# Optimization experiments

Hardware: AMD Instinct MI355X
Metric: run time of the kernel (lower is better)

The kernel has to match this reference:

```python
import jax, jax.numpy as jnp
import numpy as np

N_HEAD = 16
HEAD_DIM = 64  # n_embd // n_head = 1024 // 16

def setup_inputs() -> dict:
    key = jax.random.key(0)
    k1, k2, k3 = jax.random.split(key, 3)
    B, T, C = 4, 2048, 1024
    x = jax.random.normal(k1, (B, T, C), dtype=jnp.float32)
    w_qkv = jax.random.normal(k2, (3 * C, C), dtype=jnp.float32) * (C ** -0.5)
    w_proj = jax.random.normal(k3, (C, C), dtype=jnp.float32) * (C ** -0.5)
    b_proj = jnp.zeros((C,), dtype=jnp.float32)
    return {"x": x, "w_qkv": w_qkv, "w_proj": w_proj, "b_proj": b_proj}

def reference(x, w_qkv, w_proj, b_proj):
    B, T, C = x.shape
    H, hd = N_HEAD, HEAD_DIM
    # fused QKV projection (no bias), torch Linear: x @ W^T
    qkv = jnp.einsum('btc,dc->btd', x, w_qkv)           # [B,T,3C]
    # module-specific reshape: per-head groups of 3*hd, then chunk into q,k,v
    qkv = qkv.reshape(B, T, H, 3 * hd)
    q, k, v = jnp.split(qkv, 3, axis=-1)                # each [B,T,H,hd]
    q = q.transpose(0, 2, 1, 3)                         # [B,H,T,hd]
    k = k.transpose(0, 2, 1, 3)
    v = v.transpose(0, 2, 1, 3)
    att = jnp.einsum('bhqd,bhkd->bhqk', q, k) * (hd ** -0.5)
    causal = jnp.tril(jnp.ones((T, T), dtype=bool))
    att = jnp.where(causal, att, -jnp.inf)
    att = jax.nn.softmax(att, axis=-1)
    out = jnp.einsum('bhqk,bhkd->bhqd', att, v)         # [B,H,T,hd]
    out = out.transpose(0, 2, 1, 3).reshape(B, T, C)
    out = jnp.einsum('btc,dc->btd', out, w_proj) + b_proj
    return out
```

## Files before the change

kernel.cpp:

```cpp
#include <hip/hip_runtime.h>
#include <hip/hip_bf16.h>

typedef __attribute__((ext_vector_type(8))) short bf16x8;
typedef __attribute__((ext_vector_type(4))) float f32x4;
typedef __attribute__((ext_vector_type(16))) float f32x16;
typedef __attribute__((ext_vector_type(4))) int i32x4;
typedef unsigned short u16;

__device__ __forceinline__ u16 f2bf(float f) {
    __hip_bfloat16 h = __float2bfloat16(f);
    return __builtin_bit_cast(u16, h);
}
__device__ __forceinline__ bf16x8 load8(const u16* p) {
    return *reinterpret_cast<const bf16x8*>(p);
}
__device__ __forceinline__ void gl2lds16(const u16* g, u16* l) {
    __builtin_amdgcn_global_load_lds(
        (const __attribute__((address_space(1))) void*)g,
        (__attribute__((address_space(3))) void*)l, 16, 0, 0);
}
__device__ __forceinline__ unsigned int cvtpk(float lo, float hi) {
    unsigned int r;
    asm("v_cvt_pk_bf16_f32 %0, %1, %2" : "=v"(r) : "v"(lo), "v"(hi));
    return r;
}

#define QSCALE 0.1803368801111244f

__global__ __launch_bounds__(256) void cast_f32_bf16(
    const float* __restrict__ src, u16* __restrict__ dst, int n4)
{
    int i = blockIdx.x * blockDim.x + threadIdx.x;
    if (i < n4) {
        float4 f = reinterpret_cast<const float4*>(src)[i];
        ushort4 o;
        o.x = f2bf(f.x); o.y = f2bf(f.y); o.z = f2bf(f.z); o.w = f2bf(f.w);
        reinterpret_cast<ushort4*>(dst)[i] = o;
    }
}

#define GEMM128_BODY(EPILOGUE)                                                 \
    __shared__ __align__(16) u16 As[128 * 32];                                 \
    __shared__ __align__(16) u16 Bs[128 * 32];                                 \
    const int t = threadIdx.x;                                                 \
    const int lane = t & 63;                                                   \
    const int wave = t >> 6;                                                   \
    const int quad = lane >> 4;                                                \
    const int lid  = lane & 15;                                                \
    const int wrow = wave & 1;                                                 \
    const int wcol = wave >> 1;                                                \
    const int mtile = blockIdx.x * 128;                                        \
    const int ntile = blockIdx.y * 128;                                        \
    const int srow = t >> 2;                                                   \
    const int scol = (t & 3) * 8;                                              \
    const u16* ga0 = Aptr + (size_t)(mtile + srow) * 1024 + scol;              \
    const u16* ga1 = Aptr + (size_t)(mtile + 64 + srow) * 1024 + scol;         \
    const u16* gb0 = Bptr + (size_t)(ntile + srow) * 1024 + scol;              \
    const u16* gb1 = Bptr + (size_t)(ntile + 64 + srow) * 1024 + scol;         \
    u16* la0 = As + t * 8;                                                     \
    u16* la1 = As + (256 + t) * 8;                                             \
    u16* lb0 = Bs + t * 8;                                                     \
    u16* lb1 = Bs + (256 + t) * 8;                                             \
    f32x4 acc[4][4] = {};                                                      \
    const int aro = wrow * 64 * 32 + quad * 8;                                 \
    const int bro = wcol * 64 * 32 + quad * 8;                                 \
    for (int k0 = 0; k0 < 1024; k0 += 32) {                                    \
        __syncthreads();                                                       \
        gl2lds16(ga0 + k0, la0);                                               \
        gl2lds16(ga1 + k0, la1);                                               \
        gl2lds16(gb0 + k0, lb0);                                               \
        gl2lds16(gb1 + k0, lb1);                                               \
        __syncthreads();                                                       \
        bf16x8 a[4], b[4];                                                     \
        _Pragma("unroll")                                                      \
        for (int i = 0; i < 4; ++i) {                                          \
            a[i] = load8(As + aro + (i * 16 + lid) * 32);                      \
            b[i] = load8(Bs + bro + (i * 16 + lid) * 32);                      \
        }                                                                      \
        _Pragma("unroll")                                                      \
        for (int mi = 0; mi < 4; ++mi)                                         \
            _Pragma("unroll")                                                  \
            for (int ni = 0; ni < 4; ++ni)                                     \
                acc[mi][ni] = __builtin_amdgcn_mfma_f32_16x16x32_bf16(         \
                    a[mi], b[ni], acc[mi][ni], 0, 0, 0);                       \
    }                                                                          \
    EPILOGUE

__global__ __launch_bounds__(256) void qkv_gemm128(
    const u16* __restrict__ Aptr, const u16* __restrict__ Bptr,
    u16* __restrict__ Q, u16* __restrict__ K, u16* __restrict__ Vt)
{
    GEMM128_BODY(
    _Pragma("unroll")
    for (int mi = 0; mi < 4; ++mi)
        _Pragma("unroll")
        for (int ni = 0; ni < 4; ++ni)
            _Pragma("unroll")
            for (int r = 0; r < 4; ++r) {
                int m = mtile + wrow * 64 + mi * 16 + quad * 4 + r;
                int n = ntile + wcol * 64 + ni * 16 + lid;
                int h = n / 192;
                int rr = n - h * 192;
                int sel = rr >> 6;
                int d = rr & 63;
                float v = acc[mi][ni][r];
                if (sel == 2)
                    Vt[((size_t)h * 64 + d) * 8192 + m] = f2bf(v);
                else if (sel == 0)
                    Q[((size_t)h * 8192 + m) * 64 + d] = f2bf(v * QSCALE);
                else
                    K[((size_t)h * 8192 + m) * 64 + d] = f2bf(v);
            }
    )
}

__global__ __launch_bounds__(256) void proj_gemm128(
    const u16* __restrict__ Aptr, const u16* __restrict__ Bptr,
    const float* __restrict__ bias, float* __restrict__ out)
{
    GEMM128_BODY(
    _Pragma("unroll")
    for (int mi = 0; mi < 4; ++mi)
        _Pragma("unroll")
        for (int ni = 0; ni < 4; ++ni)
            _Pragma("unroll")
            for (int r = 0; r < 4; ++r) {
                int m = mtile + wrow * 64 + mi * 16 + quad * 4 + r;
                int n = ntile + wcol * 64 + ni * 16 + lid;
                out[(size_t)m * 1024 + n] = acc[mi][ni][r] + bias[n];
            }
    )
}

__global__ __launch_bounds__(128, 4) void attn(
    const u16* __restrict__ Q, const u16* __restrict__ K,
    const u16* __restrict__ Vtg, u16* __restrict__ O)
{
    const int qt64 = 31 - (blockIdx.x >> 6);
    const int bh = blockIdx.x & 63;
    const int b = bh >> 4, h = bh & 15;
    const int tid = threadIdx.x;
    const int lane = tid & 63;
    const int wave = tid >> 6;
    const int c31 = lane & 31;
    const int ht  = lane >> 5;

    const size_t hb = ((size_t)h * 8192 + (size_t)b * 2048) * 64;
    const u16* Qp = Q + hb;
    const u16* Kp = K + hb;
    const u16* Vp = Vtg + (size_t)h * 64 * 8192 + (size_t)b * 2048;

    __shared__ __align__(16) u16 Vt[2][64 * 64];

    const int vd = tid >> 3, vslot = tid & 7;
    const int vchunk = vslot ^ (vd & 7);
    const u16* vg = Vp + (size_t)vd * 8192 + vchunk * 8;
    u16* const ldst = (u16*)Vt[0] + vd * 64 + vslot * 8;

#define STAGE(BUFSEL, KK)                                                      \
    {                                                                          \
        u16* d_ = ldst + (BUFSEL) * 4096;                                      \
        _Pragma("unroll")                                                      \
        for (int g = 0; g < 4; ++g)                                            \
            gl2lds16(vg + (size_t)g * 16 * 8192 + (KK), d_ + g * 1024);        \
    }

    const int qw = qt64 * 64 + wave * 32;
    const int q  = qw + c31;

    bf16x8 qf[4];
#pragma unroll
    for (int dm = 0; dm < 4; ++dm)
        qf[dm] = load8(Qp + (size_t)q * 64 + dm * 16 + ht * 8);

    f32x16 od0 = {}, od1 = {};
    float lsum = 0.f;

    const int nkt = qt64 + 1;

    STAGE(0, 0)

#define SOFTMAX_KB(ST, KBOFF, PF0, PF1)                                        \
    {                                                                          \
        float pv[16];                                                          \
        _Pragma("unroll")                                                      \
        for (int r = 0; r < 16; ++r) {                                         \
            const int kg = k0 + (KBOFF) + (r & 3) + 8 * (r >> 2) + 4 * ht;     \
            float sv = ST[r];                                                  \
            if (needmask && kg > q) sv = -1e30f;                               \
            const float p = exp2f(sv);                                         \
            pv[r] = p;                                                         \
            lsum += p;                                                         \
        }                                                                      \
        _Pragma("unroll")                                                      \
        for (int a = 0; a < 2; ++a) {                                          \
            unsigned int u  = cvtpk(pv[8 * a + 0], pv[8 * a + 1]);             \
            unsigned int u2 = cvtpk(pv[8 * a + 2], pv[8 * a + 3]);             \
            unsigned int v  = cvtpk(pv[8 * a + 4], pv[8 * a + 5]);             \
            unsigned int v2 = cvtpk(pv[8 * a + 6], pv[8 * a + 7]);             \
            int r1 = __shfl_xor((int)(ht ? u : v), 32, 64);                    \
            int r2 = __shfl_xor((int)(ht ? u2 : v2), 32, 64);                  \
            i32x4 w;                                                           \
            w.x = ht ? r1 : (int)u;                                            \
            w.y = ht ? r2 : (int)u2;                                           \
            w.z = ht ? (int)v : r1;                                            \
            w.w = ht ? (int)v2 : r2;                                           \
            ((a) ? (PF1) : (PF0)) = __builtin_bit_cast(bf16x8, w);             \
        }                                                                      \
    }

    for (int kt = 0; kt < nkt; ++kt) {
        const int k0 = kt * 64;
        u16* vbuf = Vt[kt & 1];
        const bool skipB = (k0 >= qw);
        const bool needmask = (k0 + 63 > qw);
        bf16x8 pf[4];

        {
            bf16x8 kfA[4];
#pragma unroll
            for (int dm = 0; dm < 4; ++dm)
                kfA[dm] = load8(Kp + (size_t)(k0 + c31) * 64 + dm * 16 + ht * 8);
            f32x16 stA = {};
            __builtin_amdgcn_s_setprio(1);
#pragma unroll
            for (int dm = 0; dm < 4; ++dm)
                stA = __builtin_amdgcn_mfma_f32_32x32x16_bf16(kfA[dm], qf[dm], stA, 0, 0, 0);
            __builtin_amdgcn_s_setprio(0);
            SOFTMAX_KB(stA, 0, pf[0], pf[1]);
        }
        if (!skipB) {
            bf16x8 kfB[4];
#pragma unroll
            for (int dm = 0; dm < 4; ++dm)
                kfB[dm] = load8(Kp + (size_t)(k0 + 32 + c31) * 64 + dm * 16 + ht * 8);
            f32x16 stB = {};
            __builtin_amdgcn_s_setprio(1);
#pragma unroll
            for (int dm = 0; dm < 4; ++dm)
                stB = __builtin_amdgcn_mfma_f32_32x32x16_bf16(kfB[dm], qf[dm], stB, 0, 0, 0);
            __builtin_amdgcn_s_setprio(0);
            SOFTMAX_KB(stB, 32, pf[2], pf[3]);
        }

        __syncthreads();

        if (kt + 1 < nkt) STAGE((kt + 1) & 1, k0 + 64)

        __builtin_amdgcn_s_setprio(1);
#pragma unroll
        for (int km = 0; km < 4; ++km) {
            if (km >= 2 && skipB) continue;
            const int sl = ((km * 2 + ht) ^ (c31 & 7)) * 8;
            bf16x8 v0 = load8(vbuf + c31 * 64 + sl);
            bf16x8 v1 = load8(vbuf + (32 + c31) * 64 + sl);
            od0 = __builtin_amdgcn_mfma_f32_32x32x16_bf16(v0, pf[km], od0, 0, 0, 0);
            od1 = __builtin_amdgcn_mfma_f32_32x32x16_bf16(v1, pf[km], od1, 0, 0, 0);
        }
        __builtin_amdgcn_s_setprio(0);
    }

    const float tot = lsum +
        __builtin_bit_cast(float, __shfl_xor(__builtin_bit_cast(int, lsum), 32, 64));
    const float inv = 1.0f / tot;

    const size_t orow = (size_t)(b * 2048 + q) * 1024 + h * 64;
#pragma unroll
    for (int tp = 0; tp < 8; ++tp) {
        const int r = 2 * tp;
        const int d = (r & 3) + 8 * (r >> 2) + 4 * ht;
        unsigned int w0 = (unsigned int)f2bf(od0[r] * inv) |
                          ((unsigned int)f2bf(od0[r + 1] * inv) << 16);
        unsigned int w1 = (unsigned int)f2bf(od1[r] * inv) |
                          ((unsigned int)f2bf(od1[r + 1] * inv) << 16);
        *reinterpret_cast<unsigned int*>(const_cast<u16*>(O) + orow + d) = w0;
        *reinterpret_cast<unsigned int*>(const_cast<u16*>(O) + orow + 32 + d) = w1;
    }
#undef SOFTMAX_KB
#undef STAGE
}

extern "C" void kernel_launch(void* const* d_in, const int* in_sizes, int n_in,
                              void* d_out, int out_size, void* d_ws, size_t ws_size,
                              hipStream_t stream) {
    const float* x      = (const float*)d_in[0];
    const float* w_qkv  = (const float*)d_in[1];
    const float* w_proj = (const float*)d_in[2];
    const float* b_proj = (const float*)d_in[3];
    float* out = (float*)d_out;

    u16* Q   = (u16*)d_ws;
    u16* K   = Q   + (size_t)16 * 8192 * 64;
    u16* Vt  = K   + (size_t)16 * 8192 * 64;
    u16* A2  = Vt  + (size_t)16 * 64 * 8192;
    u16* Xb  = A2  + (size_t)8192 * 1024;
    u16* Wqb = Xb  + (size_t)8192 * 1024;
    u16* Wpb = Wqb + (size_t)3072 * 1024;

    cast_f32_bf16<<<dim3(8192), 256, 0, stream>>>(x, Xb, 8192 * 1024 / 4);
    cast_f32_bf16<<<dim3(3072), 256, 0, stream>>>(w_qkv, Wqb, 3072 * 1024 / 4);
    cast_f32_bf16<<<dim3(1024), 256, 0, stream>>>(w_proj, Wpb, 1024 * 1024 / 4);

    qkv_gemm128<<<dim3(64, 24), 256, 0, stream>>>(Xb, Wqb, Q, K, Vt);
    attn<<<dim3(2048), 128, 0, stream>>>(Q, K, Vt, A2);
    proj_gemm128<<<dim3(64, 8), 256, 0, stream>>>(A2, Wpb, b_proj, out);
}
```

Before: 289.2 us.

## Prefetch next K tile into registers and specialize softmax masking by template

```diff
diff --git a/kernel.cpp b/kernel.cpp
--- a/kernel.cpp
+++ b/kernel.cpp
@@ -132,6 +132,40 @@
     )
 }
 
+template<bool MASKED>
+__device__ __forceinline__ void softmax_kb(
+    const f32x16& st, int kgbase, int q, int ht, float& lsum,
+    bf16x8& pf0, bf16x8& pf1)
+{
+    float pv[16];
+#pragma unroll
+    for (int r = 0; r < 16; ++r) {
+        float sv = st[r];
+        if (MASKED) {
+            const int kg = kgbase + (r & 3) + 8 * (r >> 2);
+            if (kg > q) sv = -1e30f;
+        }
+        const float p = exp2f(sv);
+        pv[r] = p;
+        lsum += p;
+    }
+#pragma unroll
+    for (int a = 0; a < 2; ++a) {
+        unsigned int u  = cvtpk(pv[8 * a + 0], pv[8 * a + 1]);
+        unsigned int u2 = cvtpk(pv[8 * a + 2], pv[8 * a + 3]);
+        unsigned int v  = cvtpk(pv[8 * a + 4], pv[8 * a + 5]);
+        unsigned int v2 = cvtpk(pv[8 * a + 6], pv[8 * a + 7]);
+        int r1 = __shfl_xor((int)(ht ? u : v), 32, 64);
+        int r2 = __shfl_xor((int)(ht ? u2 : v2), 32, 64);
+        i32x4 w;
+        w.x = ht ? r1 : (int)u;
+        w.y = ht ? r2 : (int)u2;
+        w.z = ht ? (int)v : r1;
+        w.w = ht ? (int)v2 : r2;
+        (a ? pf1 : pf0) = __builtin_bit_cast(bf16x8, w);
+    }
+}
+
 __global__ __launch_bounds__(128, 4) void attn(
     const u16* __restrict__ Q, const u16* __restrict__ K,
     const u16* __restrict__ Vtg, u16* __restrict__ O)
@@ -179,35 +213,10 @@
     const int nkt = qt64 + 1;
 
     STAGE(0, 0)
-
-#define SOFTMAX_KB(ST, KBOFF, PF0, PF1)                                        \
-    {                                                                          \
-        float pv[16];                                                          \
-        _Pragma("unroll")                                                      \
-        for (int r = 0; r < 16; ++r) {                                         \
-            const int kg = k0 + (KBOFF) + (r & 3) + 8 * (r >> 2) + 4 * ht;     \
-            float sv = ST[r];                                                  \
-            if (needmask && kg > q) sv = -1e30f;                               \
-            const float p = exp2f(sv);                                         \
-            pv[r] = p;                                                         \
-            lsum += p;                                                         \
-        }                                                                      \
-        _Pragma("unroll")                                                      \
-        for (int a = 0; a < 2; ++a) {                                          \
-            unsigned int u  = cvtpk(pv[8 * a + 0], pv[8 * a + 1]);             \
-            unsigned int u2 = cvtpk(pv[8 * a + 2], pv[8 * a + 3]);             \
-            unsigned int v  = cvtpk(pv[8 * a + 4], pv[8 * a + 5]);             \
-            unsigned int v2 = cvtpk(pv[8 * a + 6], pv[8 * a + 7]);             \
-            int r1 = __shfl_xor((int)(ht ? u : v), 32, 64);                    \
-            int r2 = __shfl_xor((int)(ht ? u2 : v2), 32, 64);                  \
-            i32x4 w;                                                           \
-            w.x = ht ? r1 : (int)u;                                            \
-            w.y = ht ? r2 : (int)u2;                                           \
-            w.z = ht ? (int)v : r1;                                            \
-            w.w = ht ? (int)v2 : r2;                                           \
-            ((a) ? (PF1) : (PF0)) = __builtin_bit_cast(bf16x8, w);             \
-        }                                                                      \
-    }
+    bf16x8 kfAn[4];
+#pragma unroll
+    for (int dm = 0; dm < 4; ++dm)
+        kfAn[dm] = load8(Kp + (size_t)c31 * 64 + dm * 16 + ht * 8);
 
     for (int kt = 0; kt < nkt; ++kt) {
         const int k0 = kt * 64;
@@ -216,36 +225,46 @@
         const bool needmask = (k0 + 63 > qw);
         bf16x8 pf[4];
 
-        {
-            bf16x8 kfA[4];
-#pragma unroll
-            for (int dm = 0; dm < 4; ++dm)
-                kfA[dm] = load8(Kp + (size_t)(k0 + c31) * 64 + dm * 16 + ht * 8);
-            f32x16 stA = {};
-            __builtin_amdgcn_s_setprio(1);
-#pragma unroll
-            for (int dm = 0; dm < 4; ++dm)
-                stA = __builtin_amdgcn_mfma_f32_32x32x16_bf16(kfA[dm], qf[dm], stA, 0, 0, 0);
-            __builtin_amdgcn_s_setprio(0);
-            SOFTMAX_KB(stA, 0, pf[0], pf[1]);
-        }
+        bf16x8 kfB[4];
         if (!skipB) {
-            bf16x8 kfB[4];
 #pragma unroll
             for (int dm = 0; dm < 4; ++dm)
                 kfB[dm] = load8(Kp + (size_t)(k0 + 32 + c31) * 64 + dm * 16 + ht * 8);
+        }
+
+        f32x16 stA = {};
+        __builtin_amdgcn_s_setprio(1);
+#pragma unroll
+        for (int dm = 0; dm < 4; ++dm)
+            stA = __builtin_amdgcn_mfma_f32_32x32x16_bf16(kfAn[dm], qf[dm], stA, 0, 0, 0);
+        __builtin_amdgcn_s_setprio(0);
+
+        if (needmask)
+            softmax_kb<true >(stA, k0 + 4 * ht, q, ht, lsum, pf[0], pf[1]);
+        else
+            softmax_kb<false>(stA, 0, q, ht, lsum, pf[0], pf[1]);
+
+        if (!skipB) {
             f32x16 stB = {};
             __builtin_amdgcn_s_setprio(1);
 #pragma unroll
             for (int dm = 0; dm < 4; ++dm)
                 stB = __builtin_amdgcn_mfma_f32_32x32x16_bf16(kfB[dm], qf[dm], stB, 0, 0, 0);
             __builtin_amdgcn_s_setprio(0);
-            SOFTMAX_KB(stB, 32, pf[2], pf[3]);
+            if (needmask)
+                softmax_kb<true >(stB, k0 + 32 + 4 * ht, q, ht, lsum, pf[2], pf[3]);
+            else
+                softmax_kb<false>(stB, 0, q, ht, lsum, pf[2], pf[3]);
         }
 
         __syncthreads();
 
-        if (kt + 1 < nkt) STAGE((kt + 1) & 1, k0 + 64)
+        if (kt + 1 < nkt) {
+            STAGE((kt + 1) & 1, k0 + 64)
+#pragma unroll
+            for (int dm = 0; dm < 4; ++dm)
+                kfAn[dm] = load8(Kp + (size_t)(k0 + 64 + c31) * 64 + dm * 16 + ht * 8);
+        }
 
         __builtin_amdgcn_s_setprio(1);
 #pragma unroll
@@ -276,7 +295,6 @@
         *reinterpret_cast<unsigned int*>(const_cast<u16*>(O) + orow + d) = w0;
         *reinterpret_cast<unsigned int*>(const_cast<u16*>(O) + orow + 32 + d) = w1;
     }
-#undef SOFTMAX_KB
 #undef STAGE
 }
 
```

After: 296.6 us. +2.6%, slower.
